# Kernel optimization log

Measured on AMD Instinct MI355X. Metric: run time of the kernel, lower is better.

## Reference

```python
import jax, jax.numpy as jnp
import numpy as np

N = 50000      # nodes
E = 800000     # edges (avg degree 16)
IN = 512       # in_feats
HID = 64       # hidden_dim
HEADS = 4      # num_heads
NC = 40        # num_classes


def setup_inputs() -> dict:
    key = jax.random.key(0)
    ks = jax.random.split(key, 12)

    def p(k, shape, fan_in):
        return jax.random.normal(k, shape, jnp.float32) * (1.0 / np.sqrt(fan_in))

    x = jax.random.normal(ks[0], (N, IN), jnp.float32)
    edge_index = jax.random.randint(ks[1], (2, E), 0, N)
    return dict(
        x=x,
        edge_index=edge_index,
        W1=p(ks[2], (IN, HEADS * HID), IN),
        att_src1=p(ks[3], (HEADS, HID), HID),
        att_dst1=p(ks[4], (HEADS, HID), HID),
        b1=jnp.zeros((HEADS * HID,), jnp.float32),
        W2=p(ks[5], (HEADS * HID, HID), HEADS * HID),
        att_src2=p(ks[6], (1, HID), HID),
        att_dst2=p(ks[7], (1, HID), HID),
        b2=jnp.zeros((HID,), jnp.float32),
        mw1=p(ks[8], (HID, 64), HID),
        mb1=jnp.zeros((64,), jnp.float32),
        mw2=p(ks[9], (64, NC), 64),
        mb2=jnp.zeros((NC,), jnp.float32),
    )


def gat_layer(x, edge_index, W, att_src, att_dst, bias):
    # PyG GATConv with add_self_loops=False, concat=True, negative_slope=0.2
    H, C = att_src.shape
    n = x.shape[0]
    h = (x @ W).reshape(n, H, C)                       # [N,H,C]
    a_src = jnp.sum(h * att_src, axis=-1)              # [N,H]
    a_dst = jnp.sum(h * att_dst, axis=-1)              # [N,H]
    src, dst = edge_index[0], edge_index[1]
    e = jax.nn.leaky_relu(a_src[src] + a_dst[dst], 0.2)  # [E,H]
    # segment softmax grouped by destination node
    m = jax.ops.segment_max(e, dst, num_segments=n)
    ex = jnp.exp(e - m[dst])
    denom = jax.ops.segment_sum(ex, dst, num_segments=n)
    alpha = ex / (denom[dst] + 1e-16)                  # [E,H]
    out = jax.ops.segment_sum(h[src] * alpha[:, :, None], dst, num_segments=n)  # [N,H,C]
    return out.reshape(n, H * C) + bias


def reference(x, edge_index, W1, att_src1, att_dst1, b1,
              W2, att_src2, att_dst2, b2, mw1, mb1, mw2, mb2):
    h = jax.nn.elu(gat_layer(x, edge_index, W1, att_src1, att_dst1, b1))   # [N, HEADS*HID]
    emb = gat_layer(h, edge_index, W2, att_src2, att_dst2, b2)             # [N, HID] (heads=1)
    return jax.nn.relu(emb @ mw1 + mb1) @ mw2 + mb2                        # [N, NC]
```

## Files before the change

kernel.cpp:

```cpp
#include <hip/hip_runtime.h>

#define N_NODES 50000
#define N_EDGES 800000
#define SCAN_B 196

typedef short bf16x8 __attribute__((ext_vector_type(8)));
typedef short bf16x4 __attribute__((ext_vector_type(4)));
typedef float f32x4 __attribute__((ext_vector_type(4)));

#define GLDS16(g, l)                                                  \
  __builtin_amdgcn_global_load_lds(                                   \
      (const __attribute__((address_space(1))) void*)(g),             \
      (__attribute__((address_space(3))) void*)(l), 16, 0, 0)

__device__ __forceinline__ unsigned short f2bf_rne(float x) {
  unsigned u = __float_as_uint(x);
  u += 0x7FFFu + ((u >> 16) & 1u);
  return (unsigned short)(u >> 16);
}

__device__ __forceinline__ void split2(float x, short& hi, short& lo) {
  unsigned u = __float_as_uint(x);
  unsigned short h = (unsigned short)(u >> 16);
  float hf = __uint_as_float((unsigned)h << 16);
  float r = x - hf;
  unsigned short l = (unsigned short)(__float_as_uint(r) >> 16);
  hi = (short)h;
  lo = (short)l;
}

__global__ __launch_bounds__(256) void hist_k(const int* __restrict__ ei,
                                              int* __restrict__ cnt) {
  int e = blockIdx.x * 256 + threadIdx.x;
  if (e >= N_EDGES) return;
  atomicAdd(&cnt[ei[N_EDGES + e]], 1);
}

__global__ __launch_bounds__(256) void scan1(const int* __restrict__ cnt,
                                             int* __restrict__ offs,
                                             int* __restrict__ bsum) {
  __shared__ int sh[256];
  int t = threadIdx.x;
  int i = blockIdx.x * 256 + t;
  int v = (i < N_NODES) ? cnt[i] : 0;
  sh[t] = v;
  __syncthreads();
  for (int off = 1; off < 256; off <<= 1) {
    int add = (t >= off) ? sh[t - off] : 0;
    __syncthreads();
    sh[t] += add;
    __syncthreads();
  }
  if (i < N_NODES) offs[i] = sh[t] - v;
  if (t == 255) bsum[blockIdx.x] = sh[255];
}

__global__ __launch_bounds__(256) void scan2(const int* __restrict__ bsum,
                                             int* __restrict__ bofs) {
  __shared__ int sh[256];
  int t = threadIdx.x;
  int v = (t < SCAN_B) ? bsum[t] : 0;
  sh[t] = v;
  __syncthreads();
  for (int off = 1; off < 256; off <<= 1) {
    int add = (t >= off) ? sh[t - off] : 0;
    __syncthreads();
    sh[t] += add;
    __syncthreads();
  }
  if (t < SCAN_B) bofs[t] = sh[t] - v;
}

__global__ __launch_bounds__(256) void scan3(int* __restrict__ offs,
                                             const int* __restrict__ bofs) {
  int i = blockIdx.x * 256 + threadIdx.x;
  if (i < N_NODES) offs[i] += bofs[blockIdx.x];
  if (i == 0) offs[N_NODES] = N_EDGES;
}

__global__ __launch_bounds__(256) void scatter_k(const int* __restrict__ ei,
                                                 const int* __restrict__ offs,
                                                 int* __restrict__ cur,
                                                 int* __restrict__ ssort) {
  int e = blockIdx.x * 256 + threadIdx.x;
  if (e >= N_EDGES) return;
  int d = ei[N_EDGES + e];
  int p = offs[d] + atomicAdd(&cur[d], 1);
  ssort[p] = ei[e];
}

__global__ __launch_bounds__(256) void wsplit_all(
    const float* __restrict__ W1, unsigned short* __restrict__ W1h,
    unsigned short* __restrict__ W1l,
    const float* __restrict__ W2, unsigned short* __restrict__ W2h,
    unsigned short* __restrict__ W2l) {
  int i = blockIdx.x * 256 + threadIdx.x;
  const float* W;
  unsigned short *Wh, *Wl;
  int Nn, c;
  if (i < 16384) {
    W = W1; Wh = W1h; Wl = W1l; Nn = 256; c = i;
  } else if (i < 16384 + 2048) {
    W = W2; Wh = W2h; Wl = W2l; Nn = 64; c = i - 16384;
  } else {
    return;
  }
  int kq = c / Nn;
  int n = c % Nn;
  alignas(16) short h[8], l[8];
#pragma unroll
  for (int j = 0; j < 8; ++j) {
    float v = W[(size_t)(kq * 8 + j) * Nn + n];
    split2(v, h[j], l[j]);
  }
  size_t dst = (size_t)c * 8;
  *(bf16x8*)&Wh[dst] = *(bf16x8*)h;
  *(bf16x8*)&Wl[dst] = *(bf16x8*)l;
}

__global__ __launch_bounds__(256) void gemm1_fused(
    const float* __restrict__ A,
    const unsigned short* __restrict__ Bh_g, const unsigned short* __restrict__ Bl_g,
    const float* __restrict__ att_s, const float* __restrict__ att_d,
    unsigned short* __restrict__ h1b, float* __restrict__ asrc,
    float* __restrict__ adst, int M) {
  constexpr int K = 512, Nn = 256;
  constexpr int LDA = 40;
  __shared__ short Ah[128][LDA], Al[128][LDA];
  __shared__ short Bh[4 * 128 * 8], Bl[4 * 128 * 8];
  __shared__ float attLds[128][4];

  const int tid = threadIdx.x;
  const int wave = tid >> 6, lane = tid & 63;
  const int quad = lane >> 4, l16 = lane & 15;
  const int wm = (wave >> 1) * 64, wn = (wave & 1) * 64;
  const int rowBase = blockIdx.x * 128;
  const int colBase = blockIdx.y * 128;

  const int ra = tid >> 1, apart = (tid & 1) * 16;
  const int arow = min(rowBase + ra, M - 1);
  const float* aptr = A + (size_t)arow * K + apart;

  f32x4 acc[4][4] = {};

  for (int kc = 0; kc < K / 32; ++kc) {
#pragma unroll
    for (int inst = 0; inst < 2; ++inst) {
      int seq = inst * 256 + tid;
      int gq = seq >> 7, nl = seq & 127;
      size_t gsrc = (((size_t)kc * 4 + gq) * Nn + colBase + nl) * 8;
      GLDS16(Bh_g + gsrc, &Bh[seq * 8]);
      GLDS16(Bl_g + gsrc, &Bl[seq * 8]);
    }
    {
      alignas(16) short h[16], l[16];
      const float4* a4 = (const float4*)(aptr + kc * 32);
#pragma unroll
      for (int i = 0; i < 4; ++i) {
        float4 v = a4[i];
        split2(v.x, h[i * 4 + 0], l[i * 4 + 0]);
        split2(v.y, h[i * 4 + 1], l[i * 4 + 1]);
        split2(v.z, h[i * 4 + 2], l[i * 4 + 2]);
        split2(v.w, h[i * 4 + 3], l[i * 4 + 3]);
      }
      *(bf16x8*)&Ah[ra][apart]     = ((bf16x8*)h)[0];
      *(bf16x8*)&Ah[ra][apart + 8] = ((bf16x8*)h)[1];
      *(bf16x8*)&Al[ra][apart]     = ((bf16x8*)l)[0];
      *(bf16x8*)&Al[ra][apart + 8] = ((bf16x8*)l)[1];
    }
    __syncthreads();
    bf16x8 afh[4], afl[4], bfh[4], bfl[4];
#pragma unroll
    for (int mt = 0; mt < 4; ++mt) {
      afh[mt] = *(const bf16x8*)&Ah[wm + mt * 16 + l16][quad * 8];
      afl[mt] = *(const bf16x8*)&Al[wm + mt * 16 + l16][quad * 8];
    }
#pragma unroll
    for (int nt = 0; nt < 4; ++nt) {
      int bi = ((quad << 7) + wn + nt * 16 + l16) * 8;
      bfh[nt] = *(const bf16x8*)&Bh[bi];
      bfl[nt] = *(const bf16x8*)&Bl[bi];
    }
#pragma unroll
    for (int mt = 0; mt < 4; ++mt)
#pragma unroll
      for (int nt = 0; nt < 4; ++nt) {
        acc[mt][nt] = __builtin_amdgcn_mfma_f32_16x16x32_bf16(afh[mt], bfh[nt], acc[mt][nt], 0, 0, 0);
        acc[mt][nt] = __builtin_amdgcn_mfma_f32_16x16x32_bf16(afh[mt], bfl[nt], acc[mt][nt], 0, 0, 0);
        acc[mt][nt] = __builtin_amdgcn_mfma_f32_16x16x32_bf16(afl[mt], bfh[nt], acc[mt][nt], 0, 0, 0);
      }
    __syncthreads();
  }

  float asw[4], adw[4];
#pragma unroll
  for (int nt = 0; nt < 4; ++nt) {
    int c = colBase + wn + nt * 16 + l16;
    asw[nt] = att_s[c];
    adw[nt] = att_d[c];
  }
#pragma unroll
  for (int mt = 0; mt < 4; ++mt) {
    int rl = wm + mt * 16 + quad * 4;
#pragma unroll
    for (int reg = 0; reg < 4; ++reg) {
      int r = rowBase + rl + reg;
      float s = 0.f, dd = 0.f;
#pragma unroll
      for (int nt = 0; nt < 4; ++nt) {
        float v = acc[mt][nt][reg];
        s += v * asw[nt];
        dd += v * adw[nt];
        if (r < M) {
          int c = colBase + wn + nt * 16 + l16;
          h1b[(size_t)r * Nn + c] = f2bf_rne(v);
        }
      }
#pragma unroll
      for (int off = 1; off < 16; off <<= 1) {
        s += __shfl_xor(s, off);
        dd += __shfl_xor(dd, off);
      }
      if (l16 == 0) {
        attLds[rl + reg][(wn >> 6) * 2 + 0] = s;
        attLds[rl + reg][(wn >> 6) * 2 + 1] = dd;
      }
    }
  }
  __syncthreads();
  if (tid < 128) {
    int r = rowBase + tid;
    if (r < M) {
      int hb = colBase >> 6;
      asrc[r * 4 + hb + 0] = attLds[tid][0];
      adst[r * 4 + hb + 0] = attLds[tid][1];
      asrc[r * 4 + hb + 1] = attLds[tid][2];
      adst[r * 4 + hb + 1] = attLds[tid][3];
    }
  }
}

__global__ __launch_bounds__(256) void gemm2_fused(
    const float* __restrict__ A,
    const unsigned short* __restrict__ Bh_g, const unsigned short* __restrict__ Bl_g,
    const float* __restrict__ att_s, const float* __restrict__ att_d,
    unsigned short* __restrict__ h2b, float* __restrict__ asrc,
    float* __restrict__ adst, int M) {
  constexpr int K = 256, Nn = 64;
  constexpr int LDA = 40;
  __shared__ short Ah[128][LDA], Al[128][LDA];
  __shared__ short Bh[4 * 64 * 8], Bl[4 * 64 * 8];
  __shared__ float attLds[128][2];

  const int tid = threadIdx.x;
  const int wave = tid >> 6, lane = tid & 63;
  const int quad = lane >> 4, l16 = lane & 15;
  const int wm = wave * 32;
  const int rowBase = blockIdx.x * 128;

  const int ra = tid >> 1, apart = (tid & 1) * 16;
  const int arow = min(rowBase + ra, M - 1);
  const float* aptr = A + (size_t)arow * K + apart;

  f32x4 acc[2][4] = {};

  for (int kc = 0; kc < K / 32; ++kc) {
    {
      size_t gsrc = (((size_t)kc * 4) * Nn) * 8 + (size_t)tid * 8;
      GLDS16(Bh_g + gsrc, &Bh[tid * 8]);
      GLDS16(Bl_g + gsrc, &Bl[tid * 8]);
    }
    {
      alignas(16) short h[16], l[16];
      const float4* a4 = (const float4*)(aptr + kc * 32);
#pragma unroll
      for (int i = 0; i < 4; ++i) {
        float4 v = a4[i];
        split2(v.x, h[i * 4 + 0], l[i * 4 + 0]);
        split2(v.y, h[i * 4 + 1], l[i * 4 + 1]);
        split2(v.z, h[i * 4 + 2], l[i * 4 + 2]);
        split2(v.w, h[i * 4 + 3], l[i * 4 + 3]);
      }
      *(bf16x8*)&Ah[ra][apart]     = ((bf16x8*)h)[0];
      *(bf16x8*)&Ah[ra][apart + 8] = ((bf16x8*)h)[1];
      *(bf16x8*)&Al[ra][apart]     = ((bf16x8*)l)[0];
      *(bf16x8*)&Al[ra][apart + 8] = ((bf16x8*)l)[1];
    }
    __syncthreads();
    bf16x8 afh[2], afl[2], bfh[4], bfl[4];
#pragma unroll
    for (int mt = 0; mt < 2; ++mt) {
      afh[mt] = *(const bf16x8*)&Ah[wm + mt * 16 + l16][quad * 8];
      afl[mt] = *(const bf16x8*)&Al[wm + mt * 16 + l16][quad * 8];
    }
#pragma unroll
    for (int nt = 0; nt < 4; ++nt) {
      int bi = ((quad << 6) + nt * 16 + l16) * 8;
      bfh[nt] = *(const bf16x8*)&Bh[bi];
      bfl[nt] = *(const bf16x8*)&Bl[bi];
    }
#pragma unroll
    for (int mt = 0; mt < 2; ++mt)
#pragma unroll
      for (int nt = 0; nt < 4; ++nt) {
        acc[mt][nt] = __builtin_amdgcn_mfma_f32_16x16x32_bf16(afh[mt], bfh[nt], acc[mt][nt], 0, 0, 0);
        acc[mt][nt] = __builtin_amdgcn_mfma_f32_16x16x32_bf16(afh[mt], bfl[nt], acc[mt][nt], 0, 0, 0);
        acc[mt][nt] = __builtin_amdgcn_mfma_f32_16x16x32_bf16(afl[mt], bfh[nt], acc[mt][nt], 0, 0, 0);
      }
    __syncthreads();
  }

  float asw[4], adw[4];
#pragma unroll
  for (int nt = 0; nt < 4; ++nt) {
    int c = nt * 16 + l16;
    asw[nt] = att_s[c];
    adw[nt] = att_d[c];
  }
#pragma unroll
  for (int mt = 0; mt < 2; ++mt) {
    int rl = wm + mt * 16 + quad * 4;
#pragma unroll
    for (int reg = 0; reg < 4; ++reg) {
      int r = rowBase + rl + reg;
      float s = 0.f, dd = 0.f;
#pragma unroll
      for (int nt = 0; nt < 4; ++nt) {
        float v = acc[mt][nt][reg];
        s += v * asw[nt];
        dd += v * adw[nt];
        if (r < M) {
          int c = nt * 16 + l16;
          h2b[(size_t)r * Nn + c] = f2bf_rne(v);
        }
      }
#pragma unroll
      for (int off = 1; off < 16; off <<= 1) {
        s += __shfl_xor(s, off);
        dd += __shfl_xor(dd, off);
      }
      if (l16 == 0) {
        attLds[rl + reg][0] = s;
        attLds[rl + reg][1] = dd;
      }
    }
  }
  __syncthreads();
  if (tid < 128) {
    int r = rowBase + tid;
    if (r < M) {
      asrc[r] = attLds[tid][0];
      adst[r] = attLds[tid][1];
    }
  }
}

__global__ __launch_bounds__(256) void agg_l1(
    const int* __restrict__ offs, const int* __restrict__ ssort,
    const float* __restrict__ asrc, const float* __restrict__ adst,
    const unsigned short* __restrict__ h1b, const float* __restrict__ b1,
    float* __restrict__ outp, int n_nodes) {
  const int t = threadIdx.x;
  const int g = t >> 5, lt = t & 31;
  const int d = blockIdx.x * 8 + g;
  if (d >= n_nodes) return;
  const int h = lt >> 3;
  const int row0 = offs[d], row1 = offs[d + 1];
  const float ad = adst[d * 4 + h];
  float acc[8] = {};
  float denom = 0.f;
  const int m = row1 - row0;

  if (m > 0) {
    const int last = row1 - 1;
    int s0 = ssort[row0];
    int s1 = ssort[min(row0 + 1, last)];
    int s2 = ssort[min(row0 + 2, last)];
    int s3 = ssort[min(row0 + 3, last)];
    float a0 = asrc[s0 * 4 + h];
    float a1 = asrc[s1 * 4 + h];
    float a2 = asrc[s2 * 4 + h];
    bf16x8 p0 = *(const bf16x8*)&h1b[(size_t)s0 * 256 + lt * 8];
    bf16x8 p1 = *(const bf16x8*)&h1b[(size_t)s1 * 256 + lt * 8];
    bf16x8 p2 = *(const bf16x8*)&h1b[(size_t)s2 * 256 + lt * 8];
    for (int j = 0; j < m; ++j) {
      int sN = ssort[min(row0 + j + 4, last)];
      float aN = asrc[s3 * 4 + h];
      bf16x8 pN = *(const bf16x8*)&h1b[(size_t)s3 * 256 + lt * 8];
      float sc = a0 + ad;
      sc = sc > 0.f ? sc : 0.2f * sc;
      float ex = __expf(sc);
#pragma unroll
      for (int k = 0; k < 8; ++k) {
        float f = __uint_as_float((unsigned)(unsigned short)p0[k] << 16);
        acc[k] += f * ex;
      }
      denom += ex;
      s3 = sN;
      a0 = a1; a1 = a2; a2 = aN;
      p0 = p1; p1 = p2; p2 = pN;
    }
  }
  float inv = denom > 0.f ? 1.f / denom : 0.f;
  float o[8];
#pragma unroll
  for (int k = 0; k < 8; ++k) {
    float v = acc[k] * inv + b1[lt * 8 + k];
    o[k] = v > 0.f ? v : expm1f(v);
  }
  *(float4*)&outp[(size_t)d * 256 + lt * 8]     = *(float4*)&o[0];
  *(float4*)&outp[(size_t)d * 256 + lt * 8 + 4] = *(float4*)&o[4];
}

__global__ __launch_bounds__(256) void agg_l2(
    const int* __restrict__ offs, const int* __restrict__ ssort,
    const float* __restrict__ asrc, const float* __restrict__ adst,
    const unsigned short* __restrict__ h2b, const float* __restrict__ b2,
    float* __restrict__ outp, int n_nodes) {
  const int t = threadIdx.x;
  const int g = t >> 4, lt = t & 15;
  const int d = blockIdx.x * 16 + g;
  if (d >= n_nodes) return;
  const int row0 = offs[d], row1 = offs[d + 1];
  const float ad = adst[d];
  float acc[4] = {};
  float denom = 0.f;
  const int m = row1 - row0;

  if (m > 0) {
    const int last = row1 - 1;
    int s0 = ssort[row0];
    int s1 = ssort[min(row0 + 1, last)];
    int s2 = ssort[min(row0 + 2, last)];
    int s3 = ssort[min(row0 + 3, last)];
    float a0 = asrc[s0];
    float a1 = asrc[s1];
    float a2 = asrc[s2];
    bf16x4 p0 = *(const bf16x4*)&h2b[(size_t)s0 * 64 + lt * 4];
    bf16x4 p1 = *(const bf16x4*)&h2b[(size_t)s1 * 64 + lt * 4];
    bf16x4 p2 = *(const bf16x4*)&h2b[(size_t)s2 * 64 + lt * 4];
    for (int j = 0; j < m; ++j) {
      int sN = ssort[min(row0 + j + 4, last)];
      float aN = asrc[s3];
      bf16x4 pN = *(const bf16x4*)&h2b[(size_t)s3 * 64 + lt * 4];
      float sc = a0 + ad;
      sc = sc > 0.f ? sc : 0.2f * sc;
      float ex = __expf(sc);
#pragma unroll
      for (int k = 0; k < 4; ++k) {
        float f = __uint_as_float((unsigned)(unsigned short)p0[k] << 16);
        acc[k] += f * ex;
      }
      denom += ex;
      s3 = sN;
      a0 = a1; a1 = a2; a2 = aN;
      p0 = p1; p1 = p2; p2 = pN;
    }
  }
  float inv = denom > 0.f ? 1.f / denom : 0.f;
  float4 r;
  r.x = acc[0] * inv + b2[lt * 4 + 0];
  r.y = acc[1] * inv + b2[lt * 4 + 1];
  r.z = acc[2] * inv + b2[lt * 4 + 2];
  r.w = acc[3] * inv + b2[lt * 4 + 3];
  *(float4*)&outp[(size_t)d * 64 + lt * 4] = r;
}

__global__ __launch_bounds__(256) void mlp_head(
    const float* __restrict__ emb_in,
    const float* __restrict__ mw1, const float* __restrict__ mb1,
    const float* __restrict__ mw2, const float* __restrict__ mb2,
    float* __restrict__ outp, int n) {
  __shared__ float w1s[64 * 64];
  __shared__ float w2s[64 * 40];
  __shared__ float b1s[64];
  __shared__ float b2s[40];
  int t = threadIdx.x;
  for (int i = t; i < 64 * 64; i += 256) w1s[i] = mw1[i];
  for (int i = t; i < 64 * 40; i += 256) w2s[i] = mw2[i];
  if (t < 64) b1s[t] = mb1[t];
  if (t < 40) b2s[t] = mb2[t];
  __syncthreads();
  int node = blockIdx.x * 256 + t;
  if (node >= n) return;
  float emb[64];
#pragma unroll
  for (int i = 0; i < 64; ++i) emb[i] = emb_in[(size_t)node * 64 + i];
  float hid[64];
#pragma unroll
  for (int j = 0; j < 64; ++j) {
    float s = b1s[j];
#pragma unroll
    for (int i = 0; i < 64; ++i) s += emb[i] * w1s[i * 64 + j];
    hid[j] = s > 0.f ? s : 0.f;
  }
#pragma unroll
  for (int k = 0; k < 40; ++k) {
    float s = b2s[k];
#pragma unroll
    for (int j = 0; j < 64; ++j) s += hid[j] * w2s[j * 40 + k];
    outp[(size_t)node * 40 + k] = s;
  }
}

extern "C" void kernel_launch(void* const* d_in, const int* in_sizes, int n_in,
                              void* d_out, int out_size, void* d_ws, size_t ws_size,
                              hipStream_t stream) {
  const float* x        = (const float*)d_in[0];
  const int*   ei       = (const int*)d_in[1];
  const float* W1       = (const float*)d_in[2];
  const float* att_src1 = (const float*)d_in[3];
  const float* att_dst1 = (const float*)d_in[4];
  const float* b1       = (const float*)d_in[5];
  const float* W2       = (const float*)d_in[6];
  const float* att_src2 = (const float*)d_in[7];
  const float* att_dst2 = (const float*)d_in[8];
  const float* b2       = (const float*)d_in[9];
  const float* mw1      = (const float*)d_in[10];
  const float* mb1      = (const float*)d_in[11];
  const float* mw2      = (const float*)d_in[12];
  const float* mb2      = (const float*)d_in[13];
  float* out = (float*)d_out;

  const int N = N_NODES, E = N_EDGES;
  char* base = (char*)d_ws;
  size_t o = 0;
  auto alloc = [&](size_t n_elems) {
    void* p = base + o;
    o = (o + n_elems * 4 + 15) & ~(size_t)15;
    return p;
  };
  int* cnt = (int*)alloc(N);
  int* cur = (int*)alloc(N);
  size_t zero_bytes = o;
  int*   offs  = (int*)alloc(N + 2);
  int*   bsum  = (int*)alloc(256);
  int*   bofs  = (int*)alloc(256);
  int*   ssort = (int*)alloc(E);
  float* h1e   = (float*)alloc((size_t)N * 256);
  float* asrc1 = (float*)alloc((size_t)N * 4);
  float* adst1 = (float*)alloc((size_t)N * 4);
  float* emb   = (float*)alloc((size_t)N * 64);
  float* asrc2 = (float*)alloc(N);
  float* adst2 = (float*)alloc(N);
  unsigned short* h1b = (unsigned short*)alloc((size_t)N * 128);
  unsigned short* h2b = (unsigned short*)alloc((size_t)N * 32);
  unsigned short* w1h = (unsigned short*)alloc(512 * 256 / 2);
  unsigned short* w1l = (unsigned short*)alloc(512 * 256 / 2);
  unsigned short* w2h = (unsigned short*)alloc(256 * 64 / 2);
  unsigned short* w2l = (unsigned short*)alloc(256 * 64 / 2);

  hipMemsetAsync(d_ws, 0, zero_bytes, stream);

  const int EB = (E + 255) / 256;

  hist_k<<<EB, 256, 0, stream>>>(ei, cnt);
  scan1<<<SCAN_B, 256, 0, stream>>>(cnt, offs, bsum);
  scan2<<<1, 256, 0, stream>>>(bsum, bofs);
  scan3<<<SCAN_B, 256, 0, stream>>>(offs, bofs);
  scatter_k<<<EB, 256, 0, stream>>>(ei, offs, cur, ssort);
  wsplit_all<<<(16384 + 2048 + 255) / 256, 256, 0, stream>>>(W1, w1h, w1l,
                                                             W2, w2h, w2l);

  dim3 g1((N + 127) / 128, 2);
  gemm1_fused<<<g1, 256, 0, stream>>>(x, w1h, w1l, att_src1, att_dst1,
                                      h1b, asrc1, adst1, N);
  agg_l1<<<(N + 7) / 8, 256, 0, stream>>>(offs, ssort, asrc1, adst1, h1b, b1,
                                          h1e, N);

  dim3 g2((N + 127) / 128, 1);
  gemm2_fused<<<g2, 256, 0, stream>>>(h1e, w2h, w2l, att_src2, att_dst2,
                                      h2b, asrc2, adst2, N);
  agg_l2<<<(N + 15) / 16, 256, 0, stream>>>(offs, ssort, asrc2, adst2, h2b, b2,
                                            emb, N);

  mlp_head<<<(N + 255) / 256, 256, 0, stream>>>(emb, mw1, mb1, mw2, mb2, out, N);
}
```

Before: 581.8 us.

## Stage layer-1 neighbor gathers into LDS via async global_load_lds pipeline

Rewrites the layer-1 aggregation kernel so each wave handles two destination nodes and prefetches neighbor feature rows and source attention scalars three edges ahead into a 4-slot LDS ring using asynchronous global-to-LDS loads, with an explicit vmcnt wait. Source indices are loaded 32 at a time cooperatively and broadcast via shuffles instead of per-edge scalar loads. The aim is deeper memory-level parallelism on the irregular gather with less register pressure. Both half-waves now iterate to the maximum degree of the pair, masking extra work, which wastes cycles when degrees differ; the hand-tuned waitcnt count is fragile.

```diff
diff --git a/kernel.cpp b/kernel.cpp
--- a/kernel.cpp
+++ b/kernel.cpp
@@ -12,6 +12,11 @@
   __builtin_amdgcn_global_load_lds(                                   \
       (const __attribute__((address_space(1))) void*)(g),             \
       (__attribute__((address_space(3))) void*)(l), 16, 0, 0)
+
+#define GLDS4(g, l)                                                   \
+  __builtin_amdgcn_global_load_lds(                                   \
+      (const __attribute__((address_space(1))) void*)(g),             \
+      (__attribute__((address_space(3))) void*)(l), 4, 0, 0)
 
 __device__ __forceinline__ unsigned short f2bf_rne(float x) {
   unsigned u = __float_as_uint(x);
@@ -360,56 +365,84 @@
     const float* __restrict__ asrc, const float* __restrict__ adst,
     const unsigned short* __restrict__ h1b, const float* __restrict__ b1,
     float* __restrict__ outp, int n_nodes) {
+  __shared__ __align__(16) short stageP[4][4][64][8];
+  __shared__ float stageA[4][4][64];
   const int t = threadIdx.x;
-  const int g = t >> 5, lt = t & 31;
-  const int d = blockIdx.x * 8 + g;
-  if (d >= n_nodes) return;
+  const int wv = t >> 6, lane = t & 63;
+  const int lt = lane & 31;
   const int h = lt >> 3;
-  const int row0 = offs[d], row1 = offs[d + 1];
-  const float ad = adst[d * 4 + h];
+  const int d = blockIdx.x * 8 + wv * 2 + (lane >> 5);
+  const bool valid = d < n_nodes;
+  const int dc = valid ? d : n_nodes - 1;
+  const int row0 = offs[dc], row1 = offs[dc + 1];
+  const int m = valid ? (row1 - row0) : 0;
+  const float ad = adst[dc * 4 + h];
+  const int lastE = max(m, 1) - 1;
+  const int jmax = max(m, __shfl(m, lane ^ 32));
+
   float acc[8] = {};
   float denom = 0.f;
-  const int m = row1 - row0;
-
-  if (m > 0) {
-    const int last = row1 - 1;
-    int s0 = ssort[row0];
-    int s1 = ssort[min(row0 + 1, last)];
-    int s2 = ssort[min(row0 + 2, last)];
-    int s3 = ssort[min(row0 + 3, last)];
-    float a0 = asrc[s0 * 4 + h];
-    float a1 = asrc[s1 * 4 + h];
-    float a2 = asrc[s2 * 4 + h];
-    bf16x8 p0 = *(const bf16x8*)&h1b[(size_t)s0 * 256 + lt * 8];
-    bf16x8 p1 = *(const bf16x8*)&h1b[(size_t)s1 * 256 + lt * 8];
-    bf16x8 p2 = *(const bf16x8*)&h1b[(size_t)s2 * 256 + lt * 8];
-    for (int j = 0; j < m; ++j) {
-      int sN = ssort[min(row0 + j + 4, last)];
-      float aN = asrc[s3 * 4 + h];
-      bf16x8 pN = *(const bf16x8*)&h1b[(size_t)s3 * 256 + lt * 8];
-      float sc = a0 + ad;
-      sc = sc > 0.f ? sc : 0.2f * sc;
-      float ex = __expf(sc);
-#pragma unroll
-      for (int k = 0; k < 8; ++k) {
-        float f = __uint_as_float((unsigned)(unsigned short)p0[k] << 16);
-        acc[k] += f * ex;
-      }
-      denom += ex;
-      s3 = sN;
-      a0 = a1; a1 = a2; a2 = aN;
-      p0 = p1; p1 = p2; p2 = pN;
-    }
-  }
-  float inv = denom > 0.f ? 1.f / denom : 0.f;
-  float o[8];
-#pragma unroll
-  for (int k = 0; k < 8; ++k) {
-    float v = acc[k] * inv + b1[lt * 8 + k];
-    o[k] = v > 0.f ? v : expm1f(v);
-  }
-  *(float4*)&outp[(size_t)d * 256 + lt * 8]     = *(float4*)&o[0];
-  *(float4*)&outp[(size_t)d * 256 + lt * 8 + 4] = *(float4*)&o[4];
+
+  int sv0, sv1;
+  {
+    int i0 = (m > 0) ? row0 + min(lt, lastE) : 0;
+    sv0 = ssort[i0];
+    int i1 = (m > 32) ? row0 + min(32 + lt, lastE) : i0;
+    sv1 = ssort[i1];
+  }
+#pragma unroll
+  for (int jj = 0; jj < 3; ++jj) {
+    int srcl = (lane & 32) | min(jj, lastE);
+    int sjj = __shfl(sv0, srcl);
+    GLDS16(h1b + (size_t)sjj * 256 + lt * 8, &stageP[wv][jj][0][0]);
+    GLDS4(asrc + sjj * 4 + h, &stageA[wv][jj][0]);
+  }
+
+#pragma unroll 1
+  for (int j = 0; j < jmax; ++j) {
+    const int c = j >> 5;
+    if ((j & 31) == 0 && j != 0) {
+      sv0 = sv1;
+      int i1 = (m > 0) ? row0 + min((c + 1) * 32 + lt, lastE) : 0;
+      sv1 = ssort[i1];
+    }
+    int jj = j + 3;
+    int jjc = min(jj, lastE);
+    int srcl = (lane & 32) | (jjc & 31);
+    int sA = __shfl(sv0, srcl);
+    int sB = __shfl(sv1, srcl);
+    int sjj = ((jjc >> 5) == c) ? sA : sB;
+    int slot = jj & 3;
+    GLDS16(h1b + (size_t)sjj * 256 + lt * 8, &stageP[wv][slot][0][0]);
+    GLDS4(asrc + sjj * 4 + h, &stageA[wv][slot][0]);
+    __builtin_amdgcn_sched_barrier(0);
+    asm volatile("s_waitcnt vmcnt(6)" ::: "memory");
+    __builtin_amdgcn_sched_barrier(0);
+    bf16x8 p = *(const bf16x8*)&stageP[wv][j & 3][lane][0];
+    float av = stageA[wv][j & 3][lane];
+    float sc = av + ad;
+    sc = sc > 0.f ? sc : 0.2f * sc;
+    float ex = __expf(sc);
+    ex = (j < m) ? ex : 0.f;
+#pragma unroll
+    for (int k = 0; k < 8; ++k) {
+      float f = __uint_as_float((unsigned)(unsigned short)p[k] << 16);
+      acc[k] += f * ex;
+    }
+    denom += ex;
+  }
+
+  if (valid) {
+    float inv = denom > 0.f ? 1.f / denom : 0.f;
+    float o[8];
+#pragma unroll
+    for (int k = 0; k < 8; ++k) {
+      float v = acc[k] * inv + b1[lt * 8 + k];
+      o[k] = v > 0.f ? v : expm1f(v);
+    }
+    *(float4*)&outp[(size_t)d * 256 + lt * 8]     = *(float4*)&o[0];
+    *(float4*)&outp[(size_t)d * 256 + lt * 8 + 4] = *(float4*)&o[4];
+  }
 }
 
 __global__ __launch_bounds__(256) void agg_l2(
```

Measured after the change: 501.6 us. -13.8%, faster.

## Split MLP head work across 4 threads per node with LDS-staged embeddings

Applied to the files above, without the earlier changes.

The MLP head used to give each thread one whole node, which needed 64-element emb and hid arrays in registers and made strided per-thread global loads. It now handles 64 nodes per block. Embeddings are staged into padded LDS with coalesced float4 loads, and four threads each compute a quarter of the hidden and output columns, with the hidden activations passed through LDS. The aim is less register pressure, better occupancy and coalesced loads, at the cost of an extra barrier and four times as many blocks reloading the weights into LDS.

```diff
diff --git a/kernel.cpp b/kernel.cpp
--- a/kernel.cpp
+++ b/kernel.cpp
@@ -475,31 +475,58 @@
   __shared__ float w2s[64 * 40];
   __shared__ float b1s[64];
   __shared__ float b2s[40];
-  int t = threadIdx.x;
+  __shared__ float embs[64][66];
+  __shared__ float hids[64][66];
+  const int t = threadIdx.x;
   for (int i = t; i < 64 * 64; i += 256) w1s[i] = mw1[i];
   for (int i = t; i < 64 * 40; i += 256) w2s[i] = mw2[i];
   if (t < 64) b1s[t] = mb1[t];
   if (t < 40) b2s[t] = mb2[t];
+
+  const int nodeBase = blockIdx.x * 64;
+#pragma unroll
+  for (int q = 0; q < 4; ++q) {
+    int idx = q * 256 + t;
+    int nn = idx >> 4;
+    int ii = (idx & 15) * 4;
+    int gn = min(nodeBase + nn, n - 1);
+    float4 v = *(const float4*)&emb_in[(size_t)gn * 64 + ii];
+    embs[nn][ii + 0] = v.x;
+    embs[nn][ii + 1] = v.y;
+    embs[nn][ii + 2] = v.z;
+    embs[nn][ii + 3] = v.w;
+  }
   __syncthreads();
-  int node = blockIdx.x * 256 + t;
-  if (node >= n) return;
-  float emb[64];
-#pragma unroll
-  for (int i = 0; i < 64; ++i) emb[i] = emb_in[(size_t)node * 64 + i];
-  float hid[64];
-#pragma unroll
-  for (int j = 0; j < 64; ++j) {
-    float s = b1s[j];
-#pragma unroll
-    for (int i = 0; i < 64; ++i) s += emb[i] * w1s[i * 64 + j];
-    hid[j] = s > 0.f ? s : 0.f;
-  }
-#pragma unroll
-  for (int k = 0; k < 40; ++k) {
-    float s = b2s[k];
-#pragma unroll
-    for (int j = 0; j < 64; ++j) s += hid[j] * w2s[j * 40 + k];
-    outp[(size_t)node * 40 + k] = s;
+
+  const int nl = t >> 2, p = t & 3;
+  float acc[16];
+#pragma unroll
+  for (int j = 0; j < 16; ++j) acc[j] = b1s[p * 16 + j];
+  for (int i = 0; i < 64; ++i) {
+    float e = embs[nl][i];
+    const float* wrow = &w1s[i * 64 + p * 16];
+#pragma unroll
+    for (int j = 0; j < 16; ++j) acc[j] += e * wrow[j];
+  }
+#pragma unroll
+  for (int j = 0; j < 16; ++j)
+    hids[nl][p * 16 + j] = acc[j] > 0.f ? acc[j] : 0.f;
+  __syncthreads();
+
+  const int node = nodeBase + nl;
+  if (node < n) {
+    float o[10];
+#pragma unroll
+    for (int k = 0; k < 10; ++k) o[k] = b2s[p * 10 + k];
+    for (int j = 0; j < 64; ++j) {
+      float hv = hids[nl][j];
+      const float* wrow = &w2s[j * 40 + p * 10];
+#pragma unroll
+      for (int k = 0; k < 10; ++k) o[k] += hv * wrow[k];
+    }
+#pragma unroll
+    for (int k = 0; k < 10; ++k)
+      outp[(size_t)node * 40 + p * 10 + k] = o[k];
   }
 }
 
@@ -574,5 +601,5 @@
   agg_l2<<<(N + 15) / 16, 256, 0, stream>>>(offs, ssort, asrc2, adst2, h2b, b2,
                                             emb, N);
 
-  mlp_head<<<(N + 255) / 256, 256, 0, stream>>>(emb, mw1, mb1, mw2, mb2, out, N);
-}
+  mlp_head<<<(N + 63) / 64, 256, 0, stream>>>(emb, mw1, mb1, mw2, mb2, out, N);
+}
```

Measured after the change: 465.6 us. 20.0% less time.
